# Optimization experiments

Measured on AMD Instinct MI355X. Metric: run time of the kernel, lower is better.

## Reference

```python
import jax, jax.numpy as jnp
import numpy as np

B, S, D = 2, 2048, 1024
H = 16            # attention heads
KVH = 4           # key/value heads
G = H // KVH      # group_size = 4
HD = D // H       # head_dim = 64
ROPE_THETA = 10000.0


def rope(x):
    # x: [B, S, D]; interleaved-pair rotary embedding over full last dim
    d = x.shape[-1]
    inv_freq = 1.0 / (ROPE_THETA ** (jnp.arange(0, d, 2, dtype=jnp.float32) / d))  # [d/2]
    ang = jnp.arange(x.shape[1], dtype=jnp.float32)[:, None] * inv_freq[None, :]   # [S, d/2]
    cos, sin = jnp.cos(ang), jnp.sin(ang)
    x1, x2 = x[..., 0::2], x[..., 1::2]
    r1 = x1 * cos - x2 * sin
    r2 = x1 * sin + x2 * cos
    out = jnp.stack([r1, r2], axis=-1).reshape(x.shape)
    return out


def setup_inputs() -> dict:
    key = jax.random.key(0)
    kx, kq, kk, kv = jax.random.split(key, 4)
    x = jax.random.normal(kx, (B, S, D), dtype=jnp.float32)
    # mark last 256 positions of batch element 1 as padding via NaN
    x = x.at[1, S - 256:, :].set(jnp.nan)
    scale = 1.0 / np.sqrt(D)
    Wq = jax.random.normal(kq, (D, D), dtype=jnp.float32) * scale
    Wk = jax.random.normal(kk, (D, D // G), dtype=jnp.float32) * scale
    Wv = jax.random.normal(kv, (D, D // G), dtype=jnp.float32) * scale
    return {"x": x, "Wq": Wq, "Wk": Wk, "Wv": Wv}


def reference(x, Wq, Wk, Wv):
    pad = jnp.isnan(x)                      # [B,S,D]
    x = jnp.where(pad, 0.0, x)
    key_pad = jnp.any(pad, axis=-1)         # [B,S] True = padded token

    q = x @ Wq                              # [B,S,D]
    k = jnp.repeat(x @ Wk, G, axis=-1)      # grouped KV, repeat_interleave -> [B,S,D]
    v = jnp.repeat(x @ Wv, G, axis=-1)

    q = rope(q)
    k = rope(k)

    def split_heads(t):
        return t.reshape(B, S, H, HD).transpose(0, 2, 1, 3)  # [B,H,S,HD]

    q, k, v = split_heads(q), split_heads(k), split_heads(v)

    scores = jnp.einsum('bhqd,bhkd->bhqk', q, k) / np.sqrt(HD)
    causal = jnp.tril(jnp.ones((S, S), dtype=bool))
    allow = causal[None, None, :, :] & (~key_pad)[:, None, None, :]
    scores = jnp.where(allow, scores, -1e9)
    attn = jax.nn.softmax(scores, axis=-1)
    out = jnp.einsum('bhqk,bhkd->bhqd', attn, v)
    return out.transpose(0, 2, 1, 3).reshape(B, S, D)
```

## Files before the change

### kernel.cpp

```cpp
#include <hip/hip_runtime.h>
#include <hip/hip_bf16.h>
#include <math.h>

typedef unsigned short u16;
typedef unsigned int u32;
typedef __bf16 bf16x8 __attribute__((ext_vector_type(8)));
typedef float fx4 __attribute__((ext_vector_type(4)));

#define MFMA16(a, b, c) __builtin_amdgcn_mfma_f32_16x16x32_bf16(a, b, c, 0, 0, 0)

static constexpr int Bb = 2, Ss = 2048, Dd = 1024, Hh = 16, DKV = 256;
static constexpr int NQKV = 1536;
static constexpr int ROWS = Bb * Ss;
static constexpr float L2T_OVER = 0.0259525632f;
static constexpr float SC2 = 0.18033688f;
static constexpr int PSTR = 76;

__device__ __forceinline__ u16 f2bf(float f) {
    union { float f; u32 i; } v; v.f = f;
    u32 u = v.i;
    return (u16)((u + 0x7FFFu + ((u >> 16) & 1u)) >> 16);
}
__device__ __forceinline__ u16 bfr(float f) {
    return (u16)((__float_as_uint(f) + 0x8000u) >> 16);
}

__device__ __forceinline__ float fexp2(float x) {
    float r; asm("v_exp_f32 %0, %1" : "=v"(r) : "v"(x)); return r;
}
__device__ __forceinline__ void fsincos(float a, float& sn, float& cs) {
    float r = a * 0.15915494309189535f;
    r = r - floorf(r);
    asm("v_sin_f32 %0, %1" : "=v"(sn) : "v"(r));
    asm("v_cos_f32 %0, %1" : "=v"(cs) : "v"(r));
}

__device__ __forceinline__ void gl16(const u16* g, u16* l) {
    __builtin_amdgcn_global_load_lds(
        (const __attribute__((address_space(1))) void*)g,
        (__attribute__((address_space(3))) void*)l, 16, 0, 0);
}

template <int CTRL>
__device__ __forceinline__ float dppf(float x) {
    return __int_as_float(
        __builtin_amdgcn_mov_dpp(__float_as_int(x), CTRL, 0xF, 0xF, true));
}
__device__ __forceinline__ float rsum16(float x) {
    x += dppf<0xB1>(x);
    x += dppf<0x4E>(x);
    x += dppf<0x124>(x);
    x += dppf<0x128>(x);
    return x;
}

__global__ void pre_kernel(const float* __restrict__ x, const float* __restrict__ Wq,
                           const float* __restrict__ Wk, const float* __restrict__ Wv,
                           u16* __restrict__ xc, u32* __restrict__ kpb,
                           u16* __restrict__ wAll) {
    __shared__ u16 tile[32][33];
    __shared__ int flag;
    int bid = blockIdx.x, t = threadIdx.x;
    if (bid < 4096) {
        int row = bid;
        if (t == 0) flag = 0;
        __syncthreads();
        float4 d = *(const float4*)(x + (size_t)row * Dd + t * 4);
        int any = 0;
        float a0 = d.x, a1 = d.y, a2 = d.z, a3 = d.w;
        if ((__float_as_uint(a0) & 0x7FFFFFFFu) > 0x7F800000u) { a0 = 0.f; any = 1; }
        if ((__float_as_uint(a1) & 0x7FFFFFFFu) > 0x7F800000u) { a1 = 0.f; any = 1; }
        if ((__float_as_uint(a2) & 0x7FFFFFFFu) > 0x7F800000u) { a2 = 0.f; any = 1; }
        if ((__float_as_uint(a3) & 0x7FFFFFFFu) > 0x7F800000u) { a3 = 0.f; any = 1; }
        if (any) atomicOr(&flag, 1);
        uint2 o;
        o.x = (u32)f2bf(a0) | ((u32)f2bf(a1) << 16);
        o.y = (u32)f2bf(a2) | ((u32)f2bf(a3) << 16);
        *(uint2*)(xc + (size_t)row * Dd + t * 4) = o;
        __syncthreads();
        if (t == 0 && flag) {
            int b = row >> 11, s = row & (Ss - 1);
            atomicOr(&kpb[b * 64 + (s >> 5)], 1u << (s & 31));
        }
        return;
    }
    const float* in; u16* out; int C, bx, by;
    if (bid < 5120) { int i = bid - 4096; in = Wq; out = wAll; C = Dd; bx = i & 31; by = i >> 5; }
    else if (bid < 5376) { int i = bid - 5120; in = Wk; out = wAll + (size_t)Dd * Dd; C = DKV; bx = i & 7; by = i >> 3; }
    else { int i = bid - 5376; in = Wv; out = wAll + (size_t)1280 * Dd; C = DKV; bx = i & 7; by = i >> 3; }
    int c0 = bx * 32, r0 = by * 32;
    int tx = t & 31, ty = t >> 5;
    for (int i = 0; i < 32; i += 8)
        tile[ty + i][tx] = f2bf(in[(size_t)(r0 + ty + i) * C + c0 + tx]);
    __syncthreads();
    for (int i = 0; i < 32; i += 8)
        out[(size_t)(c0 + ty + i) * Dd + r0 + tx] = tile[tx][ty + i];
}

__global__ __launch_bounds__(256) void gemm_qkv(
    const u16* __restrict__ A, const u16* __restrict__ Bt, u16* __restrict__ C,
    u16* __restrict__ kr, int fuseK) {
    __shared__ __align__(16) u16 As[2][128 * 32];
    __shared__ __align__(16) u16 Bs[2][64 * 32];
    int t = threadIdx.x, w = t >> 6, lane = t & 63;
    int l15 = lane & 15, quad = lane >> 4;
    int col0 = blockIdx.x * 64, row0 = blockIdx.y * 128;
    int wm = w >> 1, wn = w & 1;
    fx4 acc[4][2];
#pragma unroll
    for (int i = 0; i < 4; ++i)
#pragma unroll
        for (int j = 0; j < 2; ++j) acc[i][j] = (fx4){0.f, 0.f, 0.f, 0.f};

    auto stage = [&](int kb, int buf) {
#pragma unroll
        for (int i = 0; i < 2; ++i) {
            int slot = i * 256 + t;
            int row = slot >> 2, p = slot & 3, g = p ^ ((row >> 1) & 3);
            gl16(A + (size_t)(row0 + row) * Dd + kb * 32 + g * 8,
                 &As[buf][(i * 256 + w * 64) * 8]);
        }
        {
            int row = t >> 2, p = t & 3, g = p ^ ((row >> 1) & 3);
            gl16(Bt + (size_t)(col0 + row) * Dd + kb * 32 + g * 8,
                 &Bs[buf][(w * 64) * 8]);
        }
    };

    stage(0, 0);
    int buf = 0;
    for (int kb = 0; kb < 32; ++kb) {
        __syncthreads();
        if (kb + 1 < 32) stage(kb + 1, buf ^ 1);
        bf16x8 af[4], bfr2[2];
#pragma unroll
        for (int mi = 0; mi < 4; ++mi) {
            int row = wm * 64 + mi * 16 + l15;
            af[mi] = *(const bf16x8*)(&As[buf][row * 32 + ((quad ^ ((row >> 1) & 3)) * 8)]);
        }
#pragma unroll
        for (int ni = 0; ni < 2; ++ni) {
            int row = wn * 32 + ni * 16 + l15;
            bfr2[ni] = *(const bf16x8*)(&Bs[buf][row * 32 + ((quad ^ ((row >> 1) & 3)) * 8)]);
        }
#pragma unroll
        for (int mi = 0; mi < 4; ++mi)
#pragma unroll
            for (int ni = 0; ni < 2; ++ni)
                acc[mi][ni] = MFMA16(af[mi], bfr2[ni], acc[mi][ni]);
        buf ^= 1;
    }

    if (fuseK && col0 >= 1024 && col0 < 1280) {
#pragma unroll
        for (int mi = 0; mi < 4; ++mi) {
            int rbase = row0 + wm * 64 + mi * 16 + quad * 4;
#pragma unroll
            for (int ni = 0; ni < 2; ++ni) {
                int tt = col0 + wn * 32 + ni * 16 + l15 - 1024;
                float f0 = fexp2(-(float)(2 * tt) * L2T_OVER);
                float f1 = fexp2(-(float)(2 * tt + 1) * L2T_OVER);
#pragma unroll
                for (int r = 0; r < 4; ++r) {
                    int row = rbase + r;
                    float pos = (float)(row & (Ss - 1));
                    float s0, c0, s1, c1;
                    fsincos(pos * f0, s0, c0);
                    fsincos(pos * f1, s1, c1);
                    float kv = acc[mi][ni][r];
                    uint2 o;
                    o.x = (u32)f2bf(kv * (c0 - s0)) | ((u32)f2bf(kv * (s0 + c0)) << 16);
                    o.y = (u32)f2bf(kv * (c1 - s1)) | ((u32)f2bf(kv * (s1 + c1)) << 16);
                    *(uint2*)(kr + (size_t)row * Dd + 4 * tt) = o;
                }
            }
        }
        return;
    }
#pragma unroll
    for (int mi = 0; mi < 4; ++mi) {
        int rbase = row0 + wm * 64 + mi * 16 + quad * 4;
#pragma unroll
        for (int ni = 0; ni < 2; ++ni) {
            int ccol = col0 + wn * 32 + ni * 16 + l15;
#pragma unroll
            for (int r = 0; r < 4; ++r)
                C[(size_t)(rbase + r) * NQKV + ccol] = f2bf(acc[mi][ni][r]);
        }
    }
}

__global__ void post_kernel(const u16* __restrict__ qkv, u16* __restrict__ kr,
                            u16* __restrict__ vtb, int ropeBlocks) {
    __shared__ u16 tile[32][33];
    int bid = blockIdx.x, t = threadIdx.x;
    if (bid < ropeBlocks) {
        int row = bid;
        float pos = (float)(row & (Ss - 1));
        float kv = __uint_as_float(((u32)qkv[(size_t)row * NQKV + Dd + t]) << 16);
        float j0 = (float)(2 * t), j1 = j0 + 1.0f;
        float f0 = fexp2(-j0 * L2T_OVER), f1 = fexp2(-j1 * L2T_OVER);
        float s0, c0, s1, c1;
        fsincos(pos * f0, s0, c0);
        fsincos(pos * f1, s1, c1);
        float r0 = kv * (c0 - s0), r1 = kv * (s0 + c0);
        float r2 = kv * (c1 - s1), r3 = kv * (s1 + c1);
        uint2 o;
        o.x = (u32)f2bf(r0) | ((u32)f2bf(r1) << 16);
        o.y = (u32)f2bf(r2) | ((u32)f2bf(r3) << 16);
        *(uint2*)(kr + (size_t)row * Dd + t * 4) = o;
        return;
    }
    int i = bid - ropeBlocks;
    int b = i >> 9, by = (i & 511) >> 3, bx = i & 7;
    int c0 = bx * 32, r0 = by * 32;
    int tx = t & 31, ty = t >> 5;
    for (int k = 0; k < 32; k += 8)
        tile[ty + k][tx] = qkv[(size_t)(b * Ss + r0 + ty + k) * NQKV + 1280 + c0 + tx];
    __syncthreads();
    for (int k = 0; k < 32; k += 8)
        vtb[(size_t)(b * DKV + c0 + ty + k) * Ss + r0 + tx] = tile[tx][ty + k];
}

__device__ __forceinline__ bf16x8 ropeFrag(uint4 raw, float pos, float jbase) {
    u32 W[4] = {raw.x, raw.y, raw.z, raw.w};
    union { u32 u[4]; bf16x8 v; } o;
#pragma unroll
    for (int c = 0; c < 4; ++c) {
        float x0 = __uint_as_float(W[c] << 16);
        float x1 = __uint_as_float(W[c] & 0xFFFF0000u);
        float f = fexp2(-(jbase + (float)c) * L2T_OVER);
        float sn, cs;
        fsincos(pos * f, sn, cs);
        float r0 = x0 * cs - x1 * sn, r1 = x0 * sn + x1 * cs;
        o.u[c] = (u32)f2bf(r0) | ((u32)f2bf(r1) << 16);
    }
    return o.v;
}

__global__ __launch_bounds__(256) void attn_kernel(
    const u16* __restrict__ qkv, const u16* __restrict__ kr,
    const u16* __restrict__ vt, const u32* __restrict__ kpb,
    float* __restrict__ O16, float* __restrict__ Lsum) {
    __shared__ __align__(16) u16 Ks[2][64 * 64];
    __shared__ __align__(16) u16 Ps[4][16 * PSTR];

    int t = threadIdx.x, w = t >> 6, lane = t & 63;
    int l15 = lane & 15, quad = lane >> 4;
    int bid = blockIdx.x;
    int u = bid >> 5, hh = bid & 31;
    int tile, c;
    if (u < 32)      { tile = 24 + (u & 7); c = u >> 3; }
    else if (u < 56) { tile = 16 + ((u - 32) & 7); c = (u - 32) >> 3; }
    else if (u < 72) { tile = 8 + ((u - 56) & 7); c = (u - 56) >> 3; }
    else             { tile = u - 72; c = 0; }
    int b = hh >> 4, h = hh & 15;
    int n = tile + 1, C = (n + 7) >> 3;
    int kb0 = (int)((u32)(n * c) / (u32)C);
    int kbe = (int)((u32)(n * (c + 1)) / (u32)C);
    int q0 = tile * 64;

    int pos = q0 + w * 16 + l15;
    const u16* qp = qkv + (size_t)(b * Ss + pos) * NQKV + h * 64;
    float jb = (float)(h * 32 + quad * 4);
    bf16x8 qf0 = ropeFrag(*(const uint4*)(qp + quad * 8), (float)pos, jb);
    bf16x8 qf1 = ropeFrag(*(const uint4*)(qp + 32 + quad * 8), (float)pos, jb + 16.f);

    u32 pw_all = kpb[b * 64 + lane];

    const u16* vrow = vt + (size_t)(b * DKV + h * 16 + l15) * Ss;

    auto stageK = [&](int k0, int buf) {
#pragma unroll
        for (int i2 = 0; i2 < 2; ++i2) {
            int row = i2 * 32 + w * 8 + (lane >> 3);
            int gg = (lane & 7) ^ (row & 7);
            gl16(kr + (size_t)(b * Ss + k0 + row) * Dd + h * 64 + gg * 8,
                 &Ks[buf][(i2 * 32 + w * 8) * 64]);
        }
    };

    float l_lane[4] = {0.f, 0.f, 0.f, 0.f};
    fx4 oacc = (fx4){0.f, 0.f, 0.f, 0.f};

    stageK(kb0 * 64, 0);
    int buf = 0;
    const int qrb = q0 + w * 16 + quad * 4;
    const int qmin = q0 + w * 16;

    for (int kb = kb0; kb < kbe; ++kb) {
        int k0 = kb * 64;
        __syncthreads();
        if (kb + 1 < kbe) stageK(k0 + 64, buf ^ 1);

        bf16x8 vf0 = *(const bf16x8*)(vrow + k0 + quad * 8);
        bf16x8 vf1 = *(const bf16x8*)(vrow + k0 + 32 + quad * 8);

        fx4 s[4];
#pragma unroll
        for (int tt = 0; tt < 4; ++tt) {
            const u16* kb_ = &Ks[buf][(tt * 16 + l15) * 64];
            bf16x8 kf0 = *(const bf16x8*)(kb_ + ((quad ^ (l15 & 7)) * 8));
            bf16x8 kf1 = *(const bf16x8*)(kb_ + (((quad + 4) ^ (l15 & 7)) * 8));
            fx4 z = (fx4){0.f, 0.f, 0.f, 0.f};
            fx4 a = MFMA16(qf0, kf0, z);
            s[tt] = MFMA16(qf1, kf1, a);
        }

        u32 pw0 = (u32)__shfl((int)pw_all, 2 * kb, 64);
        u32 pw1 = (u32)__shfl((int)pw_all, 2 * kb + 1, 64);
        bool fast = (k0 + 63 <= qmin) & ((pw0 | pw1) == 0u);

        float e[4][4];
        if (fast) {
#pragma unroll
            for (int tt = 0; tt < 4; ++tt)
#pragma unroll
                for (int r = 0; r < 4; ++r)
                    e[tt][r] = fexp2(fmaf(s[tt][r], SC2, -32.f));
        } else {
            u32 padb[4];
#pragma unroll
            for (int tt = 0; tt < 4; ++tt)
                padb[tt] = ((tt & 2 ? pw1 : pw0) >> ((tt * 16 + l15) & 31)) & 1u;
#pragma unroll
            for (int r = 0; r < 4; ++r) {
                int qq = qrb + r;
#pragma unroll
                for (int tt = 0; tt < 4; ++tt) {
                    float ee = fexp2(fmaf(s[tt][r], SC2, -32.f));
                    e[tt][r] = (k0 + tt * 16 + l15 <= qq && !padb[tt]) ? ee : 0.f;
                }
            }
        }

#pragma unroll
        for (int r = 0; r < 4; ++r) {
            l_lane[r] += (e[0][r] + e[1][r]) + (e[2][r] + e[3][r]);
            int prow = (quad * 4 + r) * PSTR + l15;
            Ps[w][prow + 0] = bfr(e[0][r]);
            Ps[w][prow + 16] = bfr(e[1][r]);
            Ps[w][prow + 32] = bfr(e[2][r]);
            Ps[w][prow + 48] = bfr(e[3][r]);
        }

        {
            bf16x8 pf0 = *(const bf16x8*)(&Ps[w][l15 * PSTR + quad * 8]);
            bf16x8 pf1 = *(const bf16x8*)(&Ps[w][l15 * PSTR + 32 + quad * 8]);
            oacc = MFMA16(pf0, vf0, oacc);
            oacc = MFMA16(pf1, vf1, oacc);
        }
        buf ^= 1;
    }

    size_t obase = (size_t)hh * Ss;
#pragma unroll
    for (int r = 0; r < 4; ++r) {
        float l_row = rsum16(l_lane[r]);
        int q = qrb + r;
        atomicAdd(&O16[(obase + q) * 16 + l15], oacc[r]);
        if (l15 == 0) atomicAdd(&Lsum[obase + q], l_row);
    }
}

__global__ void norm_kernel(const float* __restrict__ O16, const float* __restrict__ Lsum,
                            float* __restrict__ out) {
    int idx = blockIdx.x * 256 + threadIdx.x;
    int d4 = idx & 255;
    int row = idx >> 8;
    int h = d4 >> 4, f = d4 & 15;
    int b = row >> 11, s = row & (Ss - 1);
    size_t o = (size_t)(b * 16 + h) * Ss + s;
    float a = O16[o * 16 + f] / Lsum[o];
    float4 o4 = {a, a, a, a};
    *(float4*)(out + (size_t)row * Dd + d4 * 4) = o4;
}

extern "C" void kernel_launch(void* const* d_in, const int* in_sizes, int n_in,
                              void* d_out, int out_size, void* d_ws, size_t ws_size,
                              hipStream_t stream) {
    const float* x = (const float*)d_in[0];
    const float* Wq = (const float*)d_in[1];
    const float* Wk = (const float*)d_in[2];
    const float* Wv = (const float*)d_in[3];
    float* out = (float*)d_out;

    char* ws = (char*)d_ws;
    const size_t SZ_XC = (size_t)ROWS * Dd * 2;
    const size_t SZ_KPB = 4096;
    const size_t SZ_WALL = (size_t)NQKV * Dd * 2;
    const size_t SZ_QKV = (size_t)ROWS * NQKV * 2;
    const size_t SZ_O16 = (size_t)32 * Ss * 16 * 4;
    const size_t SZ_L = (size_t)32 * Ss * 4;
    const size_t SZ_KR = (size_t)ROWS * Dd * 2;

    size_t off = 0;
    u16* xc = (u16*)(ws + off); off += SZ_XC;
    u32* kpb = (u32*)(ws + off); off += SZ_KPB;
    u16* wAll = (u16*)(ws + off);
    u16* vtb = (u16*)(ws + off); off += SZ_WALL;
    u16* qkv = (u16*)(ws + off); off += SZ_QKV;
    float* O16 = (float*)(ws + off); off += SZ_O16;
    float* Ls = (float*)(ws + off); off += SZ_L;

    int fuseK = (ws_size >= off + SZ_KR) ? 1 : 0;
    u16* krope = fuseK ? (u16*)(ws + off) : xc;

    (void)in_sizes; (void)n_in; (void)out_size;

    hipMemsetAsync(kpb, 0, 1024, stream);
    hipMemsetAsync(O16, 0, SZ_O16 + SZ_L, stream);
    pre_kernel<<<5632, 256, 0, stream>>>(x, Wq, Wk, Wv, xc, kpb, wAll);
    gemm_qkv<<<dim3(NQKV / 64, ROWS / 128), 256, 0, stream>>>(xc, wAll, qkv, krope, fuseK);
    int ropeBlocks = fuseK ? 0 : 4096;
    post_kernel<<<ropeBlocks + 1024, 256, 0, stream>>>(qkv, krope, vtb, ropeBlocks);
    attn_kernel<<<2560, 256, 0, stream>>>(qkv, krope, vtb, kpb, O16, Ls);
    norm_kernel<<<4096, 256, 0, stream>>>(O16, Ls, out);
}
```

Before: 150.7 us.

## Fuse Q RoPE and V transpose into QKV GEMM epilogue, drop post kernel

The QKV GEMM epilogue now applies RoPE to Q, using a lane-swap DPP to pair adjacent columns, and writes rotated Q to its own buffer. It also writes V directly in transposed layout, so the separate post_kernel launch and the Q RoPE recomputation inside the attention kernel go away. Memsets are merged into one and the workspace is laid out statically, with no fallback path. The cost is more sincos work and strided transposed stores in the GEMM epilogue, and the code now assumes the workspace is large enough.

Result: faster. 144.4 us (-4.2%).

```diff
diff --git a/kernel.cpp b/kernel.cpp
--- a/kernel.cpp
+++ b/kernel.cpp
@@ -10,7 +10,6 @@
 #define MFMA16(a, b, c) __builtin_amdgcn_mfma_f32_16x16x32_bf16(a, b, c, 0, 0, 0)
 
 static constexpr int Bb = 2, Ss = 2048, Dd = 1024, Hh = 16, DKV = 256;
-static constexpr int NQKV = 1536;
 static constexpr int ROWS = Bb * Ss;
 static constexpr float L2T_OVER = 0.0259525632f;
 static constexpr float SC2 = 0.18033688f;
@@ -98,8 +97,8 @@
 }
 
 __global__ __launch_bounds__(256) void gemm_qkv(
-    const u16* __restrict__ A, const u16* __restrict__ Bt, u16* __restrict__ C,
-    u16* __restrict__ kr, int fuseK) {
+    const u16* __restrict__ A, const u16* __restrict__ Bt, u16* __restrict__ qbuf,
+    u16* __restrict__ kr, u16* __restrict__ vtb) {
     __shared__ __align__(16) u16 As[2][128 * 32];
     __shared__ __align__(16) u16 Bs[2][64 * 32];
     int t = threadIdx.x, w = t >> 6, lane = t & 63;
@@ -151,7 +150,29 @@
         buf ^= 1;
     }
 
-    if (fuseK && col0 >= 1024 && col0 < 1280) {
+    if (col0 < 1024) {
+        bool oddc = (l15 & 1) != 0;
+#pragma unroll
+        for (int mi = 0; mi < 4; ++mi) {
+            int rbase = row0 + wm * 64 + mi * 16 + quad * 4;
+#pragma unroll
+            for (int ni = 0; ni < 2; ++ni) {
+                int ccol = col0 + wn * 32 + ni * 16 + l15;
+                float f = fexp2(-(float)(ccol >> 1) * L2T_OVER);
+#pragma unroll
+                for (int r = 0; r < 4; ++r) {
+                    float v = acc[mi][ni][r];
+                    float p = dppf<0xB1>(v);
+                    float x0 = oddc ? p : v, x1 = oddc ? v : p;
+                    float pos = (float)((rbase + r) & (Ss - 1));
+                    float sn, cs;
+                    fsincos(pos * f, sn, cs);
+                    float res = oddc ? (x0 * sn + x1 * cs) : (x0 * cs - x1 * sn);
+                    qbuf[(size_t)(rbase + r) * Dd + ccol] = f2bf(res);
+                }
+            }
+        }
+    } else if (col0 < 1280) {
 #pragma unroll
         for (int mi = 0; mi < 4; ++mi) {
             int rbase = row0 + wm * 64 + mi * 16 + quad * 4;
@@ -175,71 +196,25 @@
                 }
             }
         }
-        return;
-    }
-#pragma unroll
-    for (int mi = 0; mi < 4; ++mi) {
-        int rbase = row0 + wm * 64 + mi * 16 + quad * 4;
-#pragma unroll
-        for (int ni = 0; ni < 2; ++ni) {
-            int ccol = col0 + wn * 32 + ni * 16 + l15;
-#pragma unroll
-            for (int r = 0; r < 4; ++r)
-                C[(size_t)(rbase + r) * NQKV + ccol] = f2bf(acc[mi][ni][r]);
-        }
-    }
-}
-
-__global__ void post_kernel(const u16* __restrict__ qkv, u16* __restrict__ kr,
-                            u16* __restrict__ vtb, int ropeBlocks) {
-    __shared__ u16 tile[32][33];
-    int bid = blockIdx.x, t = threadIdx.x;
-    if (bid < ropeBlocks) {
-        int row = bid;
-        float pos = (float)(row & (Ss - 1));
-        float kv = __uint_as_float(((u32)qkv[(size_t)row * NQKV + Dd + t]) << 16);
-        float j0 = (float)(2 * t), j1 = j0 + 1.0f;
-        float f0 = fexp2(-j0 * L2T_OVER), f1 = fexp2(-j1 * L2T_OVER);
-        float s0, c0, s1, c1;
-        fsincos(pos * f0, s0, c0);
-        fsincos(pos * f1, s1, c1);
-        float r0 = kv * (c0 - s0), r1 = kv * (s0 + c0);
-        float r2 = kv * (c1 - s1), r3 = kv * (s1 + c1);
-        uint2 o;
-        o.x = (u32)f2bf(r0) | ((u32)f2bf(r1) << 16);
-        o.y = (u32)f2bf(r2) | ((u32)f2bf(r3) << 16);
-        *(uint2*)(kr + (size_t)row * Dd + t * 4) = o;
-        return;
-    }
-    int i = bid - ropeBlocks;
-    int b = i >> 9, by = (i & 511) >> 3, bx = i & 7;
-    int c0 = bx * 32, r0 = by * 32;
-    int tx = t & 31, ty = t >> 5;
-    for (int k = 0; k < 32; k += 8)
-        tile[ty + k][tx] = qkv[(size_t)(b * Ss + r0 + ty + k) * NQKV + 1280 + c0 + tx];
-    __syncthreads();
-    for (int k = 0; k < 32; k += 8)
-        vtb[(size_t)(b * DKV + c0 + ty + k) * Ss + r0 + tx] = tile[tx][ty + k];
-}
-
-__device__ __forceinline__ bf16x8 ropeFrag(uint4 raw, float pos, float jbase) {
-    u32 W[4] = {raw.x, raw.y, raw.z, raw.w};
-    union { u32 u[4]; bf16x8 v; } o;
-#pragma unroll
-    for (int c = 0; c < 4; ++c) {
-        float x0 = __uint_as_float(W[c] << 16);
-        float x1 = __uint_as_float(W[c] & 0xFFFF0000u);
-        float f = fexp2(-(jbase + (float)c) * L2T_OVER);
-        float sn, cs;
-        fsincos(pos * f, sn, cs);
-        float r0 = x0 * cs - x1 * sn, r1 = x0 * sn + x1 * cs;
-        o.u[c] = (u32)f2bf(r0) | ((u32)f2bf(r1) << 16);
-    }
-    return o.v;
+    } else {
+#pragma unroll
+        for (int mi = 0; mi < 4; ++mi) {
+            int rbase = row0 + wm * 64 + mi * 16 + quad * 4;
+            int b = rbase >> 11, s0 = rbase & (Ss - 1);
+#pragma unroll
+            for (int ni = 0; ni < 2; ++ni) {
+                int c = col0 + wn * 32 + ni * 16 + l15 - 1280;
+                uint2 o;
+                o.x = (u32)f2bf(acc[mi][ni][0]) | ((u32)f2bf(acc[mi][ni][1]) << 16);
+                o.y = (u32)f2bf(acc[mi][ni][2]) | ((u32)f2bf(acc[mi][ni][3]) << 16);
+                *(uint2*)(vtb + (size_t)(b * DKV + c) * Ss + s0) = o;
+            }
+        }
+    }
 }
 
 __global__ __launch_bounds__(256) void attn_kernel(
-    const u16* __restrict__ qkv, const u16* __restrict__ kr,
+    const u16* __restrict__ qbuf, const u16* __restrict__ kr,
     const u16* __restrict__ vt, const u32* __restrict__ kpb,
     float* __restrict__ O16, float* __restrict__ Lsum) {
     __shared__ __align__(16) u16 Ks[2][64 * 64];
@@ -261,10 +236,9 @@
     int q0 = tile * 64;
 
     int pos = q0 + w * 16 + l15;
-    const u16* qp = qkv + (size_t)(b * Ss + pos) * NQKV + h * 64;
-    float jb = (float)(h * 32 + quad * 4);
-    bf16x8 qf0 = ropeFrag(*(const uint4*)(qp + quad * 8), (float)pos, jb);
-    bf16x8 qf1 = ropeFrag(*(const uint4*)(qp + 32 + quad * 8), (float)pos, jb + 16.f);
+    const u16* qp = qbuf + (size_t)(b * Ss + pos) * Dd + h * 64;
+    bf16x8 qf0 = *(const bf16x8*)(qp + quad * 8);
+    bf16x8 qf1 = *(const bf16x8*)(qp + 32 + quad * 8);
 
     u32 pw_all = kpb[b * 64 + lane];
 
@@ -387,33 +361,28 @@
 
     char* ws = (char*)d_ws;
     const size_t SZ_XC = (size_t)ROWS * Dd * 2;
+    const size_t SZ_WALL = (size_t)1536 * Dd * 2;
+    const size_t SZ_QB = (size_t)ROWS * Dd * 2;
+    const size_t SZ_KR = (size_t)ROWS * Dd * 2;
+    const size_t SZ_VTB = (size_t)Bb * DKV * Ss * 2;
     const size_t SZ_KPB = 4096;
-    const size_t SZ_WALL = (size_t)NQKV * Dd * 2;
-    const size_t SZ_QKV = (size_t)ROWS * NQKV * 2;
     const size_t SZ_O16 = (size_t)32 * Ss * 16 * 4;
     const size_t SZ_L = (size_t)32 * Ss * 4;
-    const size_t SZ_KR = (size_t)ROWS * Dd * 2;
 
     size_t off = 0;
     u16* xc = (u16*)(ws + off); off += SZ_XC;
+    u16* wAll = (u16*)(ws + off); off += SZ_WALL;
+    u16* qbuf = (u16*)(ws + off); off += SZ_QB;
+    u16* kr = (u16*)(ws + off); off += SZ_KR;
+    u16* vtb = (u16*)(ws + off); off += SZ_VTB;
     u32* kpb = (u32*)(ws + off); off += SZ_KPB;
-    u16* wAll = (u16*)(ws + off);
-    u16* vtb = (u16*)(ws + off); off += SZ_WALL;
-    u16* qkv = (u16*)(ws + off); off += SZ_QKV;
     float* O16 = (float*)(ws + off); off += SZ_O16;
     float* Ls = (float*)(ws + off); off += SZ_L;
-
-    int fuseK = (ws_size >= off + SZ_KR) ? 1 : 0;
-    u16* krope = fuseK ? (u16*)(ws + off) : xc;
-
-    (void)in_sizes; (void)n_in; (void)out_size;
-
-    hipMemsetAsync(kpb, 0, 1024, stream);
-    hipMemsetAsync(O16, 0, SZ_O16 + SZ_L, stream);
+    (void)ws_size; (void)in_sizes; (void)n_in; (void)out_size;
+
+    hipMemsetAsync(kpb, 0, SZ_KPB + SZ_O16 + SZ_L, stream);
     pre_kernel<<<5632, 256, 0, stream>>>(x, Wq, Wk, Wv, xc, kpb, wAll);
-    gemm_qkv<<<dim3(NQKV / 64, ROWS / 128), 256, 0, stream>>>(xc, wAll, qkv, krope, fuseK);
-    int ropeBlocks = fuseK ? 0 : 4096;
-    post_kernel<<<ropeBlocks + 1024, 256, 0, stream>>>(qkv, krope, vtb, ropeBlocks);
-    attn_kernel<<<2560, 256, 0, stream>>>(qkv, krope, vtb, kpb, O16, Ls);
+    gemm_qkv<<<dim3(1536 / 64, ROWS / 128), 256, 0, stream>>>(xc, wAll, qbuf, kr, vtb);
+    attn_kernel<<<2560, 256, 0, stream>>>(qbuf, kr, vtb, kpb, O16, Ls);
     norm_kernel<<<4096, 256, 0, stream>>>(O16, Ls, out);
 }
```
